# Kernel tuning notes

Measured on AMD Instinct MI355X. Metric: run time of the kernel, lower is better.

The kernel has to match this reference:

```python
import jax, jax.numpy as jnp
import numpy as np

B, NQ, NK, D = 4, 4096, 4096, 256


def setup_inputs() -> dict:
    key = jax.random.key(0)
    ks = jax.random.split(key, 14)
    s = 1.0 / np.sqrt(D)
    def lin(k):
        kw, kb = jax.random.split(k)
        return (jax.random.uniform(kw, (D, D), jnp.float32, -s, s),
                jax.random.uniform(kb, (D,), jnp.float32, -s, s))
    Wq, bq = lin(ks[0]); Wk, bk = lin(ks[1]); Wv, bv = lin(ks[2])
    W1, b1 = lin(ks[3]); W2, b2 = lin(ks[4]); W3, b3 = lin(ks[5])
    x = jax.random.normal(ks[6], (B, NK, D), jnp.float32)
    query = jax.random.normal(ks[7], (B, NQ, D), jnp.float32)
    return {"x": x, "query": query,
            "Wq": Wq, "bq": bq, "Wk": Wk, "bk": bk, "Wv": Wv, "bv": bv,
            "W1": W1, "b1": b1, "W2": W2, "b2": b2, "W3": W3, "b3": b3}


def reference(x, query, Wq, bq, Wk, bk, Wv, bv, W1, b1, W2, b2, W3, b3):
    # Linear: y = x @ W.T + b (torch convention)
    q = jnp.einsum('bnd,ed->bne', query, Wq) + bq   # [B,NQ,D]
    k = jnp.einsum('bnd,ed->bne', x, Wk) + bk       # [B,NK,D]
    v = jnp.einsum('bnd,ed->bne', x, Wv) + bv       # [B,NK,D]
    scale = 1.0 / jnp.sqrt(jnp.float32(x.shape[-1]))
    scores = jnp.einsum('bqd,bkd->bqk', q, k) * scale  # [B,NQ,NK]
    attn = jax.nn.softmax(scores, axis=-1)
    out = jnp.einsum('bqk,bkd->bqd', attn, v)          # [B,NQ,D]
    h = jax.nn.relu(jnp.einsum('bqd,ed->bqe', out, W1) + b1)
    h = jax.nn.relu(jnp.einsum('bqd,ed->bqe', h, W2) + b2)
    h = jax.nn.relu(jnp.einsum('bqd,ed->bqe', h, W3) + b3)
    return h, attn
```

## Files before the change

### kernel.cpp

```cpp
#include <hip/hip_runtime.h>

typedef _Float16 h16;
typedef __attribute__((ext_vector_type(4))) _Float16 h16x4;
typedef __attribute__((ext_vector_type(8))) _Float16 h16x8;
typedef __attribute__((ext_vector_type(4))) float f32x4;

#define NQD 4194304L
#define NROWS 16384L
#define NKK 4096L

static __device__ __forceinline__ f32x4 mfma16(h16x8 a, h16x8 b, f32x4 c) {
  return __builtin_amdgcn_mfma_f32_16x16x32_f16(a, b, c, 0, 0, 0);
}

__global__ void cast_weights(const float* __restrict__ w0, const float* __restrict__ w1,
                             const float* __restrict__ w2, const float* __restrict__ w3,
                             const float* __restrict__ w4, const float* __restrict__ w5,
                             h16* __restrict__ dst) {
  int wi = blockIdx.y;
  const float* src = wi == 0 ? w0 : wi == 1 ? w1 : wi == 2 ? w2 : wi == 3 ? w3 : wi == 4 ? w4 : w5;
  int c = blockIdx.x * 256 + threadIdx.x;
  float4 v = ((const float4*)src)[c];
  h16x4 h = {(h16)v.x, (h16)v.y, (h16)v.z, (h16)v.w};
  *(h16x4*)&dst[(long)wi * 65536 + (long)c * 4] = h;
}

__global__ __launch_bounds__(256) void qkv_proj(const float* __restrict__ x,
                                                const float* __restrict__ qry,
                                                const h16* __restrict__ wh,
                                                const float* __restrict__ bq,
                                                const float* __restrict__ bk,
                                                const float* __restrict__ bv,
                                                h16* __restrict__ qh,
                                                h16* __restrict__ kh,
                                                h16* __restrict__ vT) {
  const int z = blockIdx.z;
  const float* A = (z == 0) ? qry : x;
  const h16* W = wh + (long)z * 65536;
  const float* bias = (z == 0) ? bq : (z == 1) ? bk : bv;
  h16* outH = (z == 0) ? qh : (z == 1) ? kh : nullptr;
  h16* outT = (z == 2) ? vT : nullptr;

  __shared__ h16 smem[128 * 72 + 64 * 72];
  h16 (*As)[72] = (h16(*)[72])smem;
  h16 (*Bs)[72] = (h16(*)[72])(smem + 128 * 72);
  const int tid = threadIdx.x;
  const int wave = tid >> 6, lane = tid & 63;
  const int quad = lane >> 4, l16 = lane & 15;
  const long arow0 = (long)blockIdx.x * 128;
  const int bn = blockIdx.y;
  f32x4 acc[2][4] = {};
  for (int k0 = 0; k0 < 256; k0 += 64) {
    #pragma unroll
    for (int it = 0; it < 8; ++it) {
      int c = it * 256 + tid;
      int r = c >> 4, c4 = (c & 15) * 4;
      float4 v = *(const float4*)&A[(arow0 + r) * 256 + k0 + c4];
      h16x4 h = {(h16)v.x, (h16)v.y, (h16)v.z, (h16)v.w};
      *(h16x4*)&As[r][c4] = h;
    }
    #pragma unroll
    for (int it = 0; it < 2; ++it) {
      int c = it * 256 + tid;
      int r = c >> 3, c8 = (c & 7) * 8;
      *(h16x8*)&Bs[r][c8] = *(const h16x8*)&W[(long)(bn * 64 + r) * 256 + k0 + c8];
    }
    __syncthreads();
    #pragma unroll
    for (int ks = 0; ks < 64; ks += 32) {
      h16x8 a[2], b[4];
      #pragma unroll
      for (int mi = 0; mi < 2; ++mi)
        a[mi] = *(const h16x8*)&As[wave * 32 + mi * 16 + l16][ks + quad * 8];
      #pragma unroll
      for (int ni = 0; ni < 4; ++ni)
        b[ni] = *(const h16x8*)&Bs[ni * 16 + l16][ks + quad * 8];
      #pragma unroll
      for (int mi = 0; mi < 2; ++mi)
        #pragma unroll
        for (int ni = 0; ni < 4; ++ni)
          acc[mi][ni] = mfma16(a[mi], b[ni], acc[mi][ni]);
    }
    __syncthreads();
  }
  if (outH) {
    #pragma unroll
    for (int mi = 0; mi < 2; ++mi) {
      #pragma unroll
      for (int ni = 0; ni < 4; ++ni) {
        int n = bn * 64 + ni * 16 + l16;
        float bv_ = bias[n];
        #pragma unroll
        for (int i = 0; i < 4; ++i) {
          long m = arow0 + wave * 32 + mi * 16 + quad * 4 + i;
          outH[m * 256 + n] = (h16)(acc[mi][ni][i] + bv_);
        }
      }
    }
  } else {
    h16* stg = smem;
    #pragma unroll
    for (int mi = 0; mi < 2; ++mi) {
      #pragma unroll
      for (int ni = 0; ni < 4; ++ni) {
        int dl = ni * 16 + l16;
        float bv_ = bias[bn * 64 + dl];
        int mlb = wave * 32 + mi * 16 + quad * 4;
        h16x4 hv = {(h16)(acc[mi][ni][0] + bv_), (h16)(acc[mi][ni][1] + bv_),
                    (h16)(acc[mi][ni][2] + bv_), (h16)(acc[mi][ni][3] + bv_)};
        *(h16x4*)&stg[dl * 136 + mlb] = hv;
      }
    }
    __syncthreads();
    const int bb = (int)(arow0 >> 12);
    const long kb = arow0 & 4095;
    #pragma unroll
    for (int p = 0; p < 4; ++p) {
      int d = p * 16 + (tid >> 4);
      int c = (tid & 15) * 8;
      h16x8 v = *(const h16x8*)&stg[d * 136 + c];
      *(h16x8*)&outT[((long)bb * 256 + bn * 64 + d) * 4096 + kb + c] = v;
    }
  }
}

__global__ __launch_bounds__(256) void gemm256(const h16* __restrict__ A,
                                               const h16* __restrict__ W,
                                               const float* __restrict__ bias,
                                               h16* __restrict__ outH,
                                               float* __restrict__ outF) {
  __shared__ h16 As[128][72];
  __shared__ h16 Bs[64][72];
  const int tid = threadIdx.x;
  const int wave = tid >> 6, lane = tid & 63;
  const int quad = lane >> 4, l16 = lane & 15;
  const long arow0 = (long)blockIdx.x * 128;
  const int bn = blockIdx.y;
  f32x4 acc[2][4] = {};
  for (int k0 = 0; k0 < 256; k0 += 64) {
    #pragma unroll
    for (int it = 0; it < 4; ++it) {
      int c = it * 256 + tid;
      int r = c >> 3, c8 = (c & 7) * 8;
      *(h16x8*)&As[r][c8] = *(const h16x8*)&A[(arow0 + r) * 256 + k0 + c8];
    }
    #pragma unroll
    for (int it = 0; it < 2; ++it) {
      int c = it * 256 + tid;
      int r = c >> 3, c8 = (c & 7) * 8;
      *(h16x8*)&Bs[r][c8] = *(const h16x8*)&W[(long)(bn * 64 + r) * 256 + k0 + c8];
    }
    __syncthreads();
    #pragma unroll
    for (int ks = 0; ks < 64; ks += 32) {
      h16x8 a[2], b[4];
      #pragma unroll
      for (int mi = 0; mi < 2; ++mi)
        a[mi] = *(const h16x8*)&As[wave * 32 + mi * 16 + l16][ks + quad * 8];
      #pragma unroll
      for (int ni = 0; ni < 4; ++ni)
        b[ni] = *(const h16x8*)&Bs[ni * 16 + l16][ks + quad * 8];
      #pragma unroll
      for (int mi = 0; mi < 2; ++mi)
        #pragma unroll
        for (int ni = 0; ni < 4; ++ni)
          acc[mi][ni] = mfma16(a[mi], b[ni], acc[mi][ni]);
    }
    __syncthreads();
  }
  #pragma unroll
  for (int mi = 0; mi < 2; ++mi) {
    #pragma unroll
    for (int ni = 0; ni < 4; ++ni) {
      int n = bn * 64 + ni * 16 + l16;
      float bv = bias[n];
      #pragma unroll
      for (int i = 0; i < 4; ++i) {
        long m = arow0 + wave * 32 + mi * 16 + quad * 4 + i;
        float v = fmaxf(acc[mi][ni][i] + bv, 0.0f);
        if (outH) outH[m * 256 + n] = (h16)v;
        if (outF) outF[m * 256 + n] = v;
      }
    }
  }
}

__global__ __launch_bounds__(256) void gemm_scores(const h16* __restrict__ qh,
                                                   const h16* __restrict__ kh,
                                                   float2* __restrict__ stats,
                                                   h16* __restrict__ Sh,
                                                   float* __restrict__ Sf) {
  __shared__ h16 smem[128 * 72 * 2];
  h16 (*As)[72] = (h16(*)[72])smem;
  h16 (*Bs)[72] = (h16(*)[72])(smem + 128 * 72);
  const int tid = threadIdx.x;
  const int wave = tid >> 6, lane = tid & 63;
  const int quad = lane >> 4, l16 = lane & 15;
  const int bm = blockIdx.x, bn = blockIdx.y, b = blockIdx.z;
  const h16* Aq = qh + (long)b * 4096 * 256 + (long)bm * 128 * 256;
  const h16* Bk = kh + (long)b * 4096 * 256 + (long)bn * 128 * 256;
  f32x4 acc[2][8] = {};
  for (int k0 = 0; k0 < 256; k0 += 64) {
    #pragma unroll
    for (int it = 0; it < 4; ++it) {
      int c = it * 256 + tid;
      int r = c >> 3, c8 = (c & 7) * 8;
      *(h16x8*)&As[r][c8] = *(const h16x8*)&Aq[(long)r * 256 + k0 + c8];
      *(h16x8*)&Bs[r][c8] = *(const h16x8*)&Bk[(long)r * 256 + k0 + c8];
    }
    __syncthreads();
    #pragma unroll
    for (int ks = 0; ks < 64; ks += 32) {
      h16x8 a[2], bb[8];
      #pragma unroll
      for (int mi = 0; mi < 2; ++mi)
        a[mi] = *(const h16x8*)&As[wave * 32 + mi * 16 + l16][ks + quad * 8];
      #pragma unroll
      for (int ni = 0; ni < 8; ++ni)
        bb[ni] = *(const h16x8*)&Bs[ni * 16 + l16][ks + quad * 8];
      #pragma unroll
      for (int mi = 0; mi < 2; ++mi)
        #pragma unroll
        for (int ni = 0; ni < 8; ++ni)
          acc[mi][ni] = mfma16(a[mi], bb[ni], acc[mi][ni]);
    }
    __syncthreads();
  }
  #pragma unroll
  for (int mi = 0; mi < 2; ++mi)
    #pragma unroll
    for (int ni = 0; ni < 8; ++ni)
      #pragma unroll
      for (int i = 0; i < 4; ++i)
        acc[mi][ni][i] *= 0.0625f;
  #pragma unroll
  for (int mi = 0; mi < 2; ++mi) {
    #pragma unroll
    for (int i = 0; i < 4; ++i) {
      float mx = -1e30f;
      #pragma unroll
      for (int ni = 0; ni < 8; ++ni) mx = fmaxf(mx, acc[mi][ni][i]);
      #pragma unroll
      for (int off = 1; off < 16; off <<= 1) mx = fmaxf(mx, __shfl_xor(mx, off));
      float es = 0.0f;
      #pragma unroll
      for (int ni = 0; ni < 8; ++ni) es += __expf(acc[mi][ni][i] - mx);
      #pragma unroll
      for (int off = 1; off < 16; off <<= 1) es += __shfl_xor(es, off);
      if (l16 == 0) {
        long row = (long)b * 4096 + bm * 128 + wave * 32 + mi * 16 + quad * 4 + i;
        stats[row * 32 + bn] = make_float2(mx, es);
      }
    }
  }
  if (Sh) {
    h16* stg = smem;
    #pragma unroll
    for (int mi = 0; mi < 2; ++mi) {
      #pragma unroll
      for (int ni = 0; ni < 8; ++ni) {
        int c = ni * 16 + l16;
        #pragma unroll
        for (int i = 0; i < 4; ++i) {
          int r = wave * 32 + mi * 16 + quad * 4 + i;
          stg[r * 136 + c] = (h16)acc[mi][ni][i];
        }
      }
    }
    __syncthreads();
    const long rowbase = (long)b * 4096 + (long)bm * 128;
    const long colbase = (long)bn * 128;
    #pragma unroll
    for (int p = 0; p < 8; ++p) {
      int r = p * 16 + (tid >> 4);
      int c = (tid & 15) * 8;
      h16x8 v = *(const h16x8*)&stg[r * 136 + c];
      *(h16x8*)&Sh[(rowbase + r) * 4096 + colbase + c] = v;
    }
  } else {
    #pragma unroll
    for (int mi = 0; mi < 2; ++mi) {
      #pragma unroll
      for (int ni = 0; ni < 8; ++ni) {
        long col = (long)bn * 128 + ni * 16 + l16;
        #pragma unroll
        for (int i = 0; i < 4; ++i) {
          long row = (long)b * 4096 + bm * 128 + wave * 32 + mi * 16 + quad * 4 + i;
          Sf[row * 4096 + col] = acc[mi][ni][i];
        }
      }
    }
  }
}

template <typename TS>
__global__ __launch_bounds__(256, 4) void gemm_av(const TS* __restrict__ S,
                                                  const h16* __restrict__ vT,
                                                  const float2* __restrict__ stats,
                                                  float* __restrict__ attn,
                                                  float* __restrict__ Opart,
                                                  h16* __restrict__ Odirect,
                                                  int KS) {
  __shared__ h16 As[64][40];
  __shared__ h16 Bs[256][40];
  __shared__ float2 rs[64];
  const int tid = threadIdx.x;
  const int wave = tid >> 6, lane = tid & 63;
  const int quad = lane >> 4, l16 = lane & 15;
  const int mb = blockIdx.x, kc = blockIdx.y;
  const int KB = 4096 / KS;
  const long row0 = (long)mb * 64;
  const int b = mb >> 6;
  const h16* Vb = vT + (long)b * 256 * 4096;

  {
    int r = tid >> 2, j = tid & 3;
    const float2* sp = stats + (row0 + r) * 32 + j * 8;
    float2 sv[8];
    float m = -1e30f;
    #pragma unroll
    for (int t = 0; t < 8; ++t) { sv[t] = sp[t]; m = fmaxf(m, sv[t].x); }
    m = fmaxf(m, __shfl_xor(m, 1));
    m = fmaxf(m, __shfl_xor(m, 2));
    float e = 0.0f;
    #pragma unroll
    for (int t = 0; t < 8; ++t) e += sv[t].y * __expf(sv[t].x - m);
    e += __shfl_xor(e, 1);
    e += __shfl_xor(e, 2);
    if (j == 0) rs[r] = make_float2(m, 1.0f / e);
  }
  __syncthreads();

  const int sr = tid >> 2, sc = (tid & 3) * 8;
  const long srow = row0 + sr;
  const float2 st = rs[sr];
  const TS* Srow = S + srow * 4096;
  float* Arow = attn + srow * 4096;

  f32x4 acc[4][4] = {};
  const int kbeg = kc * KB, kend = kbeg + KB;
  for (int k0 = kbeg; k0 < kend; k0 += 32) {
    float p[8];
    if constexpr (sizeof(TS) == 2) {
      h16x8 sv = *(const h16x8*)&Srow[k0 + sc];
      #pragma unroll
      for (int e = 0; e < 8; ++e) p[e] = __expf((float)sv[e] - st.x) * st.y;
    } else {
      float4 sa = *(const float4*)&Srow[k0 + sc];
      float4 sb = *(const float4*)&Srow[k0 + sc + 4];
      p[0] = __expf(sa.x - st.x) * st.y; p[1] = __expf(sa.y - st.x) * st.y;
      p[2] = __expf(sa.z - st.x) * st.y; p[3] = __expf(sa.w - st.x) * st.y;
      p[4] = __expf(sb.x - st.x) * st.y; p[5] = __expf(sb.y - st.x) * st.y;
      p[6] = __expf(sb.z - st.x) * st.y; p[7] = __expf(sb.w - st.x) * st.y;
    }
    f32x4 w0 = {p[0], p[1], p[2], p[3]}, w1 = {p[4], p[5], p[6], p[7]};
    __builtin_nontemporal_store(w0, (f32x4*)&Arow[k0 + sc]);
    __builtin_nontemporal_store(w1, (f32x4*)&Arow[k0 + sc + 4]);
    h16x8 ph = {(h16)p[0], (h16)p[1], (h16)p[2], (h16)p[3],
                (h16)p[4], (h16)p[5], (h16)p[6], (h16)p[7]};
    *(h16x8*)&As[sr][sc] = ph;
    #pragma unroll
    for (int it = 0; it < 4; ++it) {
      int d = it * 64 + (tid >> 2);
      *(h16x8*)&Bs[d][sc] = *(const h16x8*)&Vb[(long)d * 4096 + k0 + sc];
    }
    __syncthreads();
    h16x8 a[4], bb[4];
    #pragma unroll
    for (int mi = 0; mi < 4; ++mi)
      a[mi] = *(const h16x8*)&As[mi * 16 + l16][quad * 8];
    #pragma unroll
    for (int ni = 0; ni < 4; ++ni)
      bb[ni] = *(const h16x8*)&Bs[wave * 64 + ni * 16 + l16][quad * 8];
    #pragma unroll
    for (int mi = 0; mi < 4; ++mi)
      #pragma unroll
      for (int ni = 0; ni < 4; ++ni)
        acc[mi][ni] = mfma16(a[mi], bb[ni], acc[mi][ni]);
    __syncthreads();
  }
  #pragma unroll
  for (int mi = 0; mi < 4; ++mi) {
    #pragma unroll
    for (int ni = 0; ni < 4; ++ni) {
      int col = wave * 64 + ni * 16 + l16;
      #pragma unroll
      for (int i = 0; i < 4; ++i) {
        long row = row0 + mi * 16 + quad * 4 + i;
        if (Opart) Opart[((long)kc * NROWS + row) * 256 + col] = acc[mi][ni][i];
        else       Odirect[row * 256 + col] = (h16)acc[mi][ni][i];
      }
    }
  }
}

__global__ __launch_bounds__(256) void reduce_O(const float* __restrict__ Opart,
                                                h16* __restrict__ oh) {
  long i4 = (long)blockIdx.x * 256 + threadIdx.x;
  float4 s = {0, 0, 0, 0};
  #pragma unroll
  for (int kc = 0; kc < 4; ++kc) {
    float4 t = *(const float4*)&Opart[kc * NQD + i4 * 4];
    s.x += t.x; s.y += t.y; s.z += t.z; s.w += t.w;
  }
  h16x4 h = {(h16)s.x, (h16)s.y, (h16)s.z, (h16)s.w};
  *(h16x4*)&oh[i4 * 4] = h;
}

extern "C" void kernel_launch(void* const* d_in, const int* in_sizes, int n_in,
                              void* d_out, int out_size, void* d_ws, size_t ws_size,
                              hipStream_t stream) {
  (void)in_sizes; (void)n_in; (void)out_size;
  const float* x   = (const float*)d_in[0];
  const float* qry = (const float*)d_in[1];
  const float* Wq  = (const float*)d_in[2];  const float* bq = (const float*)d_in[3];
  const float* Wk  = (const float*)d_in[4];  const float* bk = (const float*)d_in[5];
  const float* Wv  = (const float*)d_in[6];  const float* bv = (const float*)d_in[7];
  const float* W1  = (const float*)d_in[8];  const float* b1 = (const float*)d_in[9];
  const float* W2  = (const float*)d_in[10]; const float* b2 = (const float*)d_in[11];
  const float* W3  = (const float*)d_in[12]; const float* b3 = (const float*)d_in[13];

  float* outH = (float*)d_out;
  float* attn = outH + NQD;

  char* w = (char*)d_ws;
  h16* qh = (h16*)w;
  h16* kh = qh + NQD;
  h16* vT = kh + NQD;
  h16* oh = vT + NQD;
  h16* h1 = oh + NQD;
  h16* h2 = h1 + NQD;
  h16* wh = h2 + NQD;
  size_t off_rs   = (size_t)(6 * NQD + 6 * 65536) * 2;
  size_t BASE     = off_rs + NROWS * 8;
  size_t statsB   = NROWS * 32 * 8;
  size_t ShB      = NROWS * NKK * 2;
  size_t OpartB   = 4 * NQD * 4;

  bool modeA = ws_size >= BASE + statsB + ShB + OpartB;
  bool modeB = !modeA && ws_size >= BASE + statsB + OpartB;

  float2* stats    = (modeA || modeB) ? (float2*)(w + BASE) : (float2*)h1;
  h16*    Sh       = modeA ? (h16*)(w + BASE + statsB) : nullptr;
  float*  Opart    = modeA ? (float*)(w + BASE + statsB + ShB)
                   : modeB ? (float*)(w + BASE + statsB) : nullptr;
  int KS = (modeA || modeB) ? 4 : 1;

  cast_weights<<<dim3(64, 6), 256, 0, stream>>>(Wq, Wk, Wv, W1, W2, W3, wh);
  qkv_proj<<<dim3(128, 4, 3), 256, 0, stream>>>(x, qry, wh, bq, bk, bv, qh, kh, vT);
  gemm_scores<<<dim3(32, 32, 4), 256, 0, stream>>>(qh, kh, stats, Sh, modeA ? nullptr : attn);
  if (modeA)
    gemm_av<h16><<<dim3(256, KS), 256, 0, stream>>>(Sh, vT, stats, attn, Opart, oh, KS);
  else
    gemm_av<float><<<dim3(256, KS), 256, 0, stream>>>(attn, vT, stats, attn, Opart, oh, KS);
  if (Opart)
    reduce_O<<<dim3(4096), 256, 0, stream>>>(Opart, oh);
  gemm256<<<dim3(128, 4), 256, 0, stream>>>(oh, wh + 3 * 65536, b1, h1, nullptr);
  gemm256<<<dim3(128, 4), 256, 0, stream>>>(h1, wh + 4 * 65536, b2, h2, nullptr);
  gemm256<<<dim3(128, 4), 256, 0, stream>>>(h2, wh + 5 * 65536, b3, nullptr, outH);
}
```

Baseline: 583.6 us.

## Drop split-K in attention-V GEMM, use 512-thread blocks with register prefetch

The gemm_av kernel no longer splits the key dimension across 4 blocks. Each block now covers the full K range with 512 threads and a 64-wide K step, so the Opart fp32 partial buffer and the reduce_O kernel are gone. Global loads of the next S and V tiles are prefetched into registers while the current tile is computed. Output is staged through shared memory for coalesced fp16 stores. This cuts extra memory traffic and a launch, but only 256 blocks now run, which may leave the GPU's compute units under-filled.

```diff
diff --git a/kernel.cpp b/kernel.cpp
--- a/kernel.cpp
+++ b/kernel.cpp
@@ -294,60 +294,70 @@
 }
 
 template <typename TS>
-__global__ __launch_bounds__(256, 4) void gemm_av(const TS* __restrict__ S,
+__global__ __launch_bounds__(512, 2) void gemm_av(const TS* __restrict__ S,
                                                   const h16* __restrict__ vT,
                                                   const float2* __restrict__ stats,
                                                   float* __restrict__ attn,
-                                                  float* __restrict__ Opart,
-                                                  h16* __restrict__ Odirect,
-                                                  int KS) {
-  __shared__ h16 As[64][40];
-  __shared__ h16 Bs[256][40];
+                                                  h16* __restrict__ oh) {
+  __shared__ h16 As[64][72];
+  __shared__ h16 Bs[256][72];
   __shared__ float2 rs[64];
   const int tid = threadIdx.x;
   const int wave = tid >> 6, lane = tid & 63;
   const int quad = lane >> 4, l16 = lane & 15;
-  const int mb = blockIdx.x, kc = blockIdx.y;
-  const int KB = 4096 / KS;
+  const int mb = blockIdx.x;
   const long row0 = (long)mb * 64;
   const int b = mb >> 6;
   const h16* Vb = vT + (long)b * 256 * 4096;
 
   {
-    int r = tid >> 2, j = tid & 3;
-    const float2* sp = stats + (row0 + r) * 32 + j * 8;
-    float2 sv[8];
+    int r = tid >> 3, j = tid & 7;
+    const float2* sp = stats + (row0 + r) * 32 + j * 4;
+    float2 sv4[4];
     float m = -1e30f;
     #pragma unroll
-    for (int t = 0; t < 8; ++t) { sv[t] = sp[t]; m = fmaxf(m, sv[t].x); }
+    for (int t = 0; t < 4; ++t) { sv4[t] = sp[t]; m = fmaxf(m, sv4[t].x); }
     m = fmaxf(m, __shfl_xor(m, 1));
     m = fmaxf(m, __shfl_xor(m, 2));
+    m = fmaxf(m, __shfl_xor(m, 4));
     float e = 0.0f;
     #pragma unroll
-    for (int t = 0; t < 8; ++t) e += sv[t].y * __expf(sv[t].x - m);
+    for (int t = 0; t < 4; ++t) e += sv4[t].y * __expf(sv4[t].x - m);
     e += __shfl_xor(e, 1);
     e += __shfl_xor(e, 2);
+    e += __shfl_xor(e, 4);
     if (j == 0) rs[r] = make_float2(m, 1.0f / e);
   }
   __syncthreads();
 
-  const int sr = tid >> 2, sc = (tid & 3) * 8;
+  const int sr = tid >> 3, sc = (tid & 7) * 8;
   const long srow = row0 + sr;
   const float2 st = rs[sr];
   const TS* Srow = S + srow * 4096;
   float* Arow = attn + srow * 4096;
-
-  f32x4 acc[4][4] = {};
-  const int kbeg = kc * KB, kend = kbeg + KB;
-  for (int k0 = kbeg; k0 < kend; k0 += 32) {
+  const int vd = tid >> 3;
+
+  f32x4 acc[4][2] = {};
+
+  h16x8 sv; float4 sa, sb;
+  h16x8 bv0, bv1, bv2, bv3;
+  if constexpr (sizeof(TS) == 2) {
+    sv = *(const h16x8*)&Srow[sc];
+  } else {
+    sa = *(const float4*)&Srow[sc];
+    sb = *(const float4*)&Srow[sc + 4];
+  }
+  bv0 = *(const h16x8*)&Vb[(long)(vd)       * 4096 + sc];
+  bv1 = *(const h16x8*)&Vb[(long)(vd + 64)  * 4096 + sc];
+  bv2 = *(const h16x8*)&Vb[(long)(vd + 128) * 4096 + sc];
+  bv3 = *(const h16x8*)&Vb[(long)(vd + 192) * 4096 + sc];
+
+  for (int k0 = 0; k0 < 4096; k0 += 64) {
     float p[8];
     if constexpr (sizeof(TS) == 2) {
-      h16x8 sv = *(const h16x8*)&Srow[k0 + sc];
       #pragma unroll
       for (int e = 0; e < 8; ++e) p[e] = __expf((float)sv[e] - st.x) * st.y;
     } else {
-      float4 sa = *(const float4*)&Srow[k0 + sc];
-      float4 sb = *(const float4*)&Srow[k0 + sc + 4];
       p[0] = __expf(sa.x - st.x) * st.y; p[1] = __expf(sa.y - st.x) * st.y;
       p[2] = __expf(sa.z - st.x) * st.y; p[3] = __expf(sa.w - st.x) * st.y;
       p[4] = __expf(sb.x - st.x) * st.y; p[5] = __expf(sb.y - st.x) * st.y;
@@ -359,52 +369,63 @@
     h16x8 ph = {(h16)p[0], (h16)p[1], (h16)p[2], (h16)p[3],
                 (h16)p[4], (h16)p[5], (h16)p[6], (h16)p[7]};
     *(h16x8*)&As[sr][sc] = ph;
-    #pragma unroll
-    for (int it = 0; it < 4; ++it) {
-      int d = it * 64 + (tid >> 2);
-      *(h16x8*)&Bs[d][sc] = *(const h16x8*)&Vb[(long)d * 4096 + k0 + sc];
-    }
-    __syncthreads();
-    h16x8 a[4], bb[4];
-    #pragma unroll
-    for (int mi = 0; mi < 4; ++mi)
-      a[mi] = *(const h16x8*)&As[mi * 16 + l16][quad * 8];
-    #pragma unroll
-    for (int ni = 0; ni < 4; ++ni)
-      bb[ni] = *(const h16x8*)&Bs[wave * 64 + ni * 16 + l16][quad * 8];
-    #pragma unroll
-    for (int mi = 0; mi < 4; ++mi)
-      #pragma unroll
-      for (int ni = 0; ni < 4; ++ni)
-        acc[mi][ni] = mfma16(a[mi], bb[ni], acc[mi][ni]);
-    __syncthreads();
-  }
+    *(h16x8*)&Bs[vd][sc]       = bv0;
+    *(h16x8*)&Bs[vd + 64][sc]  = bv1;
+    *(h16x8*)&Bs[vd + 128][sc] = bv2;
+    *(h16x8*)&Bs[vd + 192][sc] = bv3;
+    int kn = k0 + 64;
+    if (kn < 4096) {
+      if constexpr (sizeof(TS) == 2) {
+        sv = *(const h16x8*)&Srow[kn + sc];
+      } else {
+        sa = *(const float4*)&Srow[kn + sc];
+        sb = *(const float4*)&Srow[kn + sc + 4];
+      }
+      bv0 = *(const h16x8*)&Vb[(long)(vd)       * 4096 + kn + sc];
+      bv1 = *(const h16x8*)&Vb[(long)(vd + 64)  * 4096 + kn + sc];
+      bv2 = *(const h16x8*)&Vb[(long)(vd + 128) * 4096 + kn + sc];
+      bv3 = *(const h16x8*)&Vb[(long)(vd + 192) * 4096 + kn + sc];
+    }
+    __syncthreads();
+    #pragma unroll
+    for (int ks = 0; ks < 64; ks += 32) {
+      h16x8 a[4], bb[2];
+      #pragma unroll
+      for (int mi = 0; mi < 4; ++mi)
+        a[mi] = *(const h16x8*)&As[mi * 16 + l16][ks + quad * 8];
+      #pragma unroll
+      for (int ni = 0; ni < 2; ++ni)
+        bb[ni] = *(const h16x8*)&Bs[wave * 32 + ni * 16 + l16][ks + quad * 8];
+      #pragma unroll
+      for (int mi = 0; mi < 4; ++mi)
+        #pragma unroll
+        for (int ni = 0; ni < 2; ++ni)
+          acc[mi][ni] = mfma16(a[mi], bb[ni], acc[mi][ni]);
+    }
+    __syncthreads();
+  }
+  h16* stg = &Bs[0][0];
+  const int SW = 264;
   #pragma unroll
   for (int mi = 0; mi < 4; ++mi) {
     #pragma unroll
-    for (int ni = 0; ni < 4; ++ni) {
-      int col = wave * 64 + ni * 16 + l16;
+    for (int ni = 0; ni < 2; ++ni) {
+      int col = wave * 32 + ni * 16 + l16;
       #pragma unroll
       for (int i = 0; i < 4; ++i) {
-        long row = row0 + mi * 16 + quad * 4 + i;
-        if (Opart) Opart[((long)kc * NROWS + row) * 256 + col] = acc[mi][ni][i];
-        else       Odirect[row * 256 + col] = (h16)acc[mi][ni][i];
-      }
-    }
-  }
-}
-
-__global__ __launch_bounds__(256) void reduce_O(const float* __restrict__ Opart,
-                                                h16* __restrict__ oh) {
-  long i4 = (long)blockIdx.x * 256 + threadIdx.x;
-  float4 s = {0, 0, 0, 0};
+        int r = mi * 16 + quad * 4 + i;
+        stg[r * SW + col] = (h16)acc[mi][ni][i];
+      }
+    }
+  }
+  __syncthreads();
   #pragma unroll
-  for (int kc = 0; kc < 4; ++kc) {
-    float4 t = *(const float4*)&Opart[kc * NQD + i4 * 4];
-    s.x += t.x; s.y += t.y; s.z += t.z; s.w += t.w;
-  }
-  h16x4 h = {(h16)s.x, (h16)s.y, (h16)s.z, (h16)s.w};
-  *(h16x4*)&oh[i4 * 4] = h;
+  for (int p = 0; p < 4; ++p) {
+    int r = tid >> 3;
+    int c = (tid & 7) * 8 + p * 64;
+    h16x8 v = *(const h16x8*)&stg[r * SW + c];
+    *(h16x8*)&oh[(row0 + r) * 256 + c] = v;
+  }
 }
 
 extern "C" void kernel_launch(void* const* d_in, const int* in_sizes, int n_in,
@@ -435,26 +456,20 @@
   size_t BASE     = off_rs + NROWS * 8;
   size_t statsB   = NROWS * 32 * 8;
   size_t ShB      = NROWS * NKK * 2;
-  size_t OpartB   = 4 * NQD * 4;
-
-  bool modeA = ws_size >= BASE + statsB + ShB + OpartB;
-  bool modeB = !modeA && ws_size >= BASE + statsB + OpartB;
-
-  float2* stats    = (modeA || modeB) ? (float2*)(w + BASE) : (float2*)h1;
-  h16*    Sh       = modeA ? (h16*)(w + BASE + statsB) : nullptr;
-  float*  Opart    = modeA ? (float*)(w + BASE + statsB + ShB)
-                   : modeB ? (float*)(w + BASE + statsB) : nullptr;
-  int KS = (modeA || modeB) ? 4 : 1;
+
+  bool modeA = ws_size >= BASE + statsB + ShB;
+  bool modeB = !modeA && ws_size >= BASE + statsB;
+
+  float2* stats = (modeA || modeB) ? (float2*)(w + BASE) : (float2*)h1;
+  h16*    Sh    = modeA ? (h16*)(w + BASE + statsB) : nullptr;
 
   cast_weights<<<dim3(64, 6), 256, 0, stream>>>(Wq, Wk, Wv, W1, W2, W3, wh);
   qkv_proj<<<dim3(128, 4, 3), 256, 0, stream>>>(x, qry, wh, bq, bk, bv, qh, kh, vT);
   gemm_scores<<<dim3(32, 32, 4), 256, 0, stream>>>(qh, kh, stats, Sh, modeA ? nullptr : attn);
   if (modeA)
-    gemm_av<h16><<<dim3(256, KS), 256, 0, stream>>>(Sh, vT, stats, attn, Opart, oh, KS);
+    gemm_av<h16><<<dim3(256), 512, 0, stream>>>(Sh, vT, stats, attn, oh);
   else
-    gemm_av<float><<<dim3(256, KS), 256, 0, stream>>>(attn, vT, stats, attn, Opart, oh, KS);
-  if (Opart)
-    reduce_O<<<dim3(4096), 256, 0, stream>>>(Opart, oh);
+    gemm_av<float><<<dim3(256), 512, 0, stream>>>(attn, vT, stats, attn, oh);
   gemm256<<<dim3(128, 4), 256, 0, stream>>>(oh, wh + 3 * 65536, b1, h1, nullptr);
   gemm256<<<dim3(128, 4), 256, 0, stream>>>(h1, wh + 4 * 65536, b2, h2, nullptr);
   gemm256<<<dim3(128, 4), 256, 0, stream>>>(h2, wh + 5 * 65536, b3, nullptr, outH);
```

Result: faster. 550.3 us (-5.7%).
